# Optimization experiments

Hardware: AMD Instinct MI355X
Metric: run time of the kernel (lower is better)

Reference implementation:

```python
import jax, jax.numpy as jnp
import numpy as np

B, C, N = 2, 128, 4096
BN_EPS = 1e-5


def setup_inputs() -> dict:
    key = jax.random.key(0)
    ks = jax.random.split(key, 16)
    Ch, Cd = C // 2, C // 8

    def bn_params(k1, c):
        k1, k2 = jax.random.split(k1)
        return (1.0 + 0.1 * jax.random.normal(k1, (c,), jnp.float32),  # gamma
                0.1 * jax.random.normal(k2, (c,), jnp.float32),        # beta
                jnp.zeros((c,), jnp.float32),                          # running mean
                jnp.ones((c,), jnp.float32))                           # running var

    g1, be1, m1, v1 = bn_params(ks[4], Ch)
    g2, be2, m2, v2 = bn_params(ks[5], Ch)
    gu, beu, mu, vu = bn_params(ks[6], C)
    return {
        "xyz": jax.random.normal(ks[0], (B, 3, N), jnp.float32),
        "features": jax.random.normal(ks[1], (B, C, N), jnp.float32),
        "w_mlp1": 0.1 * jax.random.normal(ks[2], (Ch, 6), jnp.float32),
        "b_mlp1": jnp.zeros((Ch,), jnp.float32),
        "g_mlp1": g1, "be_mlp1": be1, "m_mlp1": m1, "v_mlp1": v1,
        "w_mlp2": 0.05 * jax.random.normal(ks[3], (Ch, 2 * C), jnp.float32),
        "b_mlp2": jnp.zeros((Ch,), jnp.float32),
        "g_mlp2": g2, "be_mlp2": be2, "m_mlp2": m2, "v_mlp2": v2,
        "w_down1": 0.1 * jax.random.normal(ks[7], (Cd, C), jnp.float32),
        "w_down2": 0.1 * jax.random.normal(ks[8], (Cd, C), jnp.float32),
        "w_up": 0.1 * jax.random.normal(ks[9], (C, Cd), jnp.float32),
        "b_up": jnp.zeros((C,), jnp.float32),
        "g_up": gu, "be_up": beu, "m_up": mu, "v_up": vu,
        "k": 20,
    }


def _knn_idx(x, k):
    # x: [B,3,N]; pairwise_distance = -||xi-xj||^2, topk -> nearest
    xx = jnp.sum(x * x, axis=1)                       # [B,N]
    inner = jnp.einsum('bcn,bcm->bnm', x, x)          # [B,N,N]
    pd = 2.0 * inner - xx[:, :, None] - xx[:, None, :]
    return jax.lax.top_k(pd, k)[1]                    # [B,N,k]


def _gather_edge(feat_t, idx):
    # feat_t: [B,N,C], idx: [B,N,k] -> concat(nbr - center, center): [B,N,k,2C]
    nbr = jax.vmap(lambda a, i: a[i])(feat_t, idx)    # [B,N,k,C]
    center = feat_t[:, :, None, :]
    center_b = jnp.broadcast_to(center, nbr.shape)
    return jnp.concatenate((nbr - center, center_b), axis=-1)


def _bn(x, g, b, m, v, ch_axis=1):
    shape = [1] * x.ndim
    shape[ch_axis] = -1
    r = lambda p: p.reshape(shape)
    return (x - r(m)) * (r(g) / jnp.sqrt(r(v) + BN_EPS)) + r(b)


def reference(xyz, features, w_mlp1, b_mlp1, g_mlp1, be_mlp1, m_mlp1, v_mlp1,
              w_mlp2, b_mlp2, g_mlp2, be_mlp2, m_mlp2, v_mlp2,
              w_down1, w_down2, w_up, b_up, g_up, be_up, m_up, v_up, k):
    idx = _knn_idx(xyz, k)
    edge_x = _gather_edge(jnp.swapaxes(xyz, 1, 2), idx)        # [B,N,k,6]
    edge_f = _gather_edge(jnp.swapaxes(features, 1, 2), idx)   # [B,N,k,2C]

    # 1x1 conv2d + BN + ReLU on both branches (channels last via einsum)
    h1 = jnp.einsum('bnkc,oc->bonk', edge_x, w_mlp1) + b_mlp1[None, :, None, None]
    h1 = jax.nn.relu(_bn(h1, g_mlp1, be_mlp1, m_mlp1, v_mlp1))
    h2 = jnp.einsum('bnkc,oc->bonk', edge_f, w_mlp2) + b_mlp2[None, :, None, None]
    h2 = jax.nn.relu(_bn(h2, g_mlp2, be_mlp2, m_mlp2, v_mlp2))

    f_enc = jnp.max(jnp.concatenate((h1, h2), axis=1), axis=-1)  # [B,C,N]

    f1 = jax.nn.relu(jnp.einsum('bcn,oc->bon', f_enc, w_down1))  # [B,C/8,N]
    f2 = jax.nn.relu(jnp.einsum('bcn,oc->bon', f_enc, w_down2))

    # NOTE: original code indexes [0] after mean -> uses batch element 0 only
    f_channel = jnp.mean(f1, axis=-1, keepdims=True)[0]          # [C/8,1]
    f_space = jnp.mean(f2, axis=1, keepdims=True)[0]             # [1,N]
    final = jnp.sqrt(f_channel @ f_space + 1e-12)                # [C/8,N]
    final = final[None] + f1 + f2                                # [B,C/8,N]

    up = jnp.einsum('bcn,oc->bon', final, w_up) + b_up[None, :, None]
    final = jax.nn.relu(_bn(up, g_up, be_up, m_up, v_up))        # [B,C,N]

    f_local = f_enc - final
    return f_local * jnp.tanh(jax.nn.softplus(f_local))          # Mish
```

## Files before the change

### kernel.cpp

```cpp
#include <hip/hip_runtime.h>
#include <hip/hip_bf16.h>

#define BB 2
#define CC 128
#define NN 4096
#define KK 20

#define WS_FLAG   0
#define WS_FCACC  16
#define WS_S1     32
#define WS_C1     96
#define WS_S2     160
#define WS_C2     224
#define WS_SUP    288
#define WS_CUP    416
#define WS_FS     1024
#define WS_X      8192
#define WS_XX     32768
#define WS_W1     40960
#define WS_W2     41344
#define WS_WD1    57728
#define WS_WD2    59776
#define WS_WUP    61824
#define WS_P      65536
#define WS_Q      1114112
#define WS_FE     2326528
#define WS_F      WS_FE
#define WS_F12    3375104

struct InPtrs { const void* p[22]; };

__device__ __forceinline__ int detect_bf16(const void* xyz) {
  const unsigned* u = (const unsigned*)xyz;
  int cnt = 0;
  for (int i = 0; i < 64; ++i) {
    unsigned lo = u[i] & 0x7FFFu;
    cnt += (lo >= 0x3C00u && lo <= 0x4100u) ? 1 : 0;
  }
  return cnt >= 32;
}

__device__ __forceinline__ float ldin(const void* p, long long i, int flag) {
  if (flag) {
    unsigned short b = ((const unsigned short*)p)[i];
    return __uint_as_float(((unsigned)b) << 16);
  }
  return ((const float*)p)[i];
}

__device__ __forceinline__ unsigned sortable(float v) {
  unsigned u = __float_as_uint(v);
  return (u & 0x80000000u) ? ~u : (u | 0x80000000u);
}

__device__ __forceinline__ unsigned wave_max_u32(unsigned x) {
  unsigned t;
  t = (unsigned)__builtin_amdgcn_update_dpp(0, (int)x, 0x111, 0xF, 0xF, true); x = x > t ? x : t;
  t = (unsigned)__builtin_amdgcn_update_dpp(0, (int)x, 0x112, 0xF, 0xF, true); x = x > t ? x : t;
  t = (unsigned)__builtin_amdgcn_update_dpp(0, (int)x, 0x114, 0xF, 0xF, true); x = x > t ? x : t;
  t = (unsigned)__builtin_amdgcn_update_dpp(0, (int)x, 0x118, 0xF, 0xF, true); x = x > t ? x : t;
  t = (unsigned)__builtin_amdgcn_update_dpp(0, (int)x, 0x142, 0xF, 0xF, true); x = x > t ? x : t;
  t = (unsigned)__builtin_amdgcn_update_dpp(0, (int)x, 0x143, 0xF, 0xF, true); x = x > t ? x : t;
  return (unsigned)__builtin_amdgcn_readlane((int)x, 63);
}

__device__ __forceinline__ void insert4p(unsigned pd, int idx,
    unsigned& p0, int& i0, unsigned& p1, int& i1,
    unsigned& p2, int& i2, unsigned& p3, int& i3) {
  bool b0 = pd > p0, b1 = pd > p1, b2 = pd > p2, b3 = pd > p3;
  p3 = b3 ? (b2 ? p2 : pd) : p3;  i3 = b3 ? (b2 ? i2 : idx) : i3;
  p2 = b2 ? (b1 ? p1 : pd) : p2;  i2 = b2 ? (b1 ? i1 : idx) : i2;
  p1 = b1 ? (b0 ? p0 : pd) : p1;  i1 = b1 ? (b0 ? i0 : idx) : i1;
  p0 = b0 ? pd : p0;              i0 = b0 ? idx : i0;
}

__global__ __launch_bounds__(256) void k0_convert(InPtrs in, float* ws) {
  int flag = detect_bf16(in.p[0]);
  int gid = blockIdx.x * 256 + threadIdx.x;
  int stride = gridDim.x * 256;
  if (flag) {
    const ushort4* src = (const ushort4*)in.p[1];
    float4* dst = (float4*)(ws + WS_F);
    for (int i = gid; i < 262144; i += stride) {
      ushort4 s = src[i];
      dst[i] = make_float4(
        __uint_as_float(((unsigned)s.x) << 16), __uint_as_float(((unsigned)s.y) << 16),
        __uint_as_float(((unsigned)s.z) << 16), __uint_as_float(((unsigned)s.w) << 16));
    }
  } else {
    const float4* src = (const float4*)in.p[1];
    float4* dst = (float4*)(ws + WS_F);
    for (int i = gid; i < 262144; i += stride) dst[i] = src[i];
  }
  const int T0 = 24576;
  const int T1 = T0 + 384;
  const int T2 = T1 + 16384;
  const int T3 = T2 + 2048;
  const int T4 = T3 + 2048;
  const int T5 = T4 + 2048;
  for (int i = gid; i < T5; i += stride) {
    const void* src; int off, dst;
    if      (i < T0) { src = in.p[0];  off = i;      dst = WS_X   + off; }
    else if (i < T1) { src = in.p[2];  off = i - T0; dst = WS_W1  + off; }
    else if (i < T2) { src = in.p[8];  off = i - T1; dst = WS_W2  + off; }
    else if (i < T3) { src = in.p[14]; off = i - T2; dst = WS_WD1 + off; }
    else if (i < T4) { src = in.p[15]; off = i - T3; dst = WS_WD2 + off; }
    else             { src = in.p[16]; off = i - T4; dst = WS_WUP + off; }
    ws[dst] = ldin(src, off, flag);
  }
  if (blockIdx.x == 0) {
    int t = threadIdx.x;
    if (t < 64) {
      float b1 = ldin(in.p[3], t, flag), g1 = ldin(in.p[4], t, flag);
      float be1 = ldin(in.p[5], t, flag), m1 = ldin(in.p[6], t, flag), v1 = ldin(in.p[7], t, flag);
      float s1 = g1 / sqrtf(v1 + 1e-5f);
      ws[WS_S1 + t] = s1;
      ws[WS_C1 + t] = s1 * (b1 - m1) + be1;
      float b2 = ldin(in.p[9], t, flag), g2 = ldin(in.p[10], t, flag);
      float be2 = ldin(in.p[11], t, flag), m2 = ldin(in.p[12], t, flag), v2 = ldin(in.p[13], t, flag);
      float s2 = g2 / sqrtf(v2 + 1e-5f);
      ws[WS_S2 + t] = s2;
      ws[WS_C2 + t] = s2 * (b2 - m2) + be2;
    }
    if (t < 128) {
      float bu = ldin(in.p[17], t, flag), gu = ldin(in.p[18], t, flag);
      float beu = ldin(in.p[19], t, flag), mu = ldin(in.p[20], t, flag), vu = ldin(in.p[21], t, flag);
      float su = gu / sqrtf(vu + 1e-5f);
      ws[WS_SUP + t] = su;
      ws[WS_CUP + t] = su * (bu - mu) + beu;
    }
    if (t < 16) ws[WS_FCACC + t] = 0.f;
    if (t == 0) ((int*)ws)[WS_FLAG] = flag;
  }
}

__global__ __launch_bounds__(256) void k1_pq(float* ws) {
  __shared__ float ldsW[64 * 128];
  __shared__ float ldsF[64 * 32];
  int t = threadIdx.x;
  int bid = blockIdx.x;
  int b = bid >> 7;
  int m0 = (bid & 127) << 5;
  int w = t >> 6, sub = (t >> 5) & 1, mloc = t & 31;
  const float* F = ws + WS_F + (long long)b * CC * NN;
  const float* W2 = ws + WS_W2;
  float accP[8], accQ[8];
#pragma unroll
  for (int j = 0; j < 8; ++j) { accP[j] = 0.f; accQ[j] = 0.f; }
  for (int half = 0; half < 2; ++half) {
    if (half) __syncthreads();
    for (int i = t; i < 64 * 128; i += 256) {
      int o = i >> 7, r = i & 127;
      int c = (r & 63) + half * 64 + ((r >> 6) << 7);
      ldsW[i] = W2[o * 256 + c];
    }
    for (int i = t; i < 64 * 32; i += 256) {
      int cl = i >> 5, ml = i & 31;
      ldsF[i] = F[(long long)(half * 64 + cl) * NN + m0 + ml];
    }
    __syncthreads();
    for (int cl = 0; cl < 64; ++cl) {
      float f = ldsF[cl * 32 + mloc];
#pragma unroll
      for (int j = 0; j < 8; ++j) {
        int o = w * 16 + sub * 8 + j;
        accP[j] = fmaf(ldsW[o * 128 + cl], f, accP[j]);
        accQ[j] = fmaf(ldsW[o * 128 + 64 + cl], f, accQ[j]);
      }
    }
  }
  int m = m0 + mloc;
  const float* X = ws + WS_X + (long long)b * 3 * NN;
  float x0 = X[m], x1 = X[NN + m], x2 = X[2 * NN + m];
  const float* W1 = ws + WS_W1;
  float* P = ws + WS_P + ((long long)(b * NN + m)) * 128;
  float* Q = ws + WS_Q + ((long long)(b * NN + m)) * 128;
#pragma unroll
  for (int j = 0; j < 8; ++j) {
    int o = w * 16 + sub * 8 + j;
    float s1 = ws[WS_S1 + o], c1 = ws[WS_C1 + o];
    float px = fmaf(W1[o * 6 + 2], x2, fmaf(W1[o * 6 + 1], x1, W1[o * 6 + 0] * x0));
    float qx = fmaf(W1[o * 6 + 5], x2, fmaf(W1[o * 6 + 4], x1, W1[o * 6 + 3] * x0));
    P[o] = s1 * px;
    Q[o] = fmaf(s1, qx - px, c1);
    float s2 = ws[WS_S2 + o], c2 = ws[WS_C2 + o];
    P[64 + o] = s2 * accP[j];
    Q[64 + o] = fmaf(s2, accQ[j] - accP[j], c2);
  }
  if (t < 32) {
    float xx = __fadd_rn(__fadd_rn(__fmul_rn(x0, x0), __fmul_rn(x1, x1)), __fmul_rn(x2, x2));
    ws[WS_XX + b * NN + m] = xx;
  }
}

__global__ __launch_bounds__(256) void k23_knn_fenc(float* ws) {
  int t = threadIdx.x;
  int w = t >> 6, lane = t & 63;
  int pt = blockIdx.x * 4 + w;
  int b = pt >> 12;
  int n = pt & (NN - 1);
  const float* X = ws + WS_X + (long long)b * 3 * NN;
  const float* XX = ws + WS_XX + (long long)b * NN;
  float xc0 = X[n], xc1 = X[NN + n], xc2 = X[2 * NN + n], xxn = XX[n];
  unsigned p0 = 0, p1 = 0, p2 = 0, p3 = 0;
  int i0 = 0, i1 = 0, i2 = 0, i3 = 0;
#pragma unroll 4
  for (int s = 0; s < 64; ++s) {
    int m = s * 64 + lane;
    float c0 = X[m], c1 = X[NN + m], c2 = X[2 * NN + m], xxm = XX[m];
    float inner = __fadd_rn(__fadd_rn(__fmul_rn(c0, xc0), __fmul_rn(c1, xc1)), __fmul_rn(c2, xc2));
    float pd = __fsub_rn(__fsub_rn(__fmul_rn(2.0f, inner), xxn), xxm);
    insert4p(sortable(pd), m, p0, i0, p1, i1, p2, i2, p3, i3);
  }
  unsigned long long used = 0;
  int nv = 4;
  int winner = 0;
  for (int r = 0; r < KK; ++r) {
    unsigned spd = wave_max_u32(p0);
    unsigned cand = (p0 == spd) ? (unsigned)(4095 - i0) : 0u;
    unsigned sidx = 4095u - wave_max_u32(cand);
    if (lane == r) winner = (int)sidx;
    if (p0 == spd && i0 == (int)sidx) {
      used |= 1ull << (i0 >> 6);
      p0 = p1; i0 = i1; p1 = p2; i1 = i2; p2 = p3; i2 = i3; p3 = 0; i3 = 0;
      if (--nv == 0) {
        p0 = p1 = p2 = p3 = 0; i0 = i1 = i2 = i3 = 0;
#pragma unroll 1
        for (int s = 0; s < 64; ++s) {
          if (!((used >> s) & 1ull)) {
            int m = s * 64 + lane;
            float c0 = X[m], c1 = X[NN + m], c2 = X[2 * NN + m], xxm = XX[m];
            float inner = __fadd_rn(__fadd_rn(__fmul_rn(c0, xc0), __fmul_rn(c1, xc1)), __fmul_rn(c2, xc2));
            float pd = __fsub_rn(__fsub_rn(__fmul_rn(2.0f, inner), xxn), xxm);
            insert4p(sortable(pd), m, p0, i0, p1, i1, p2, i2, p3, i3);
          }
        }
        nv = 4;
      }
    }
  }
  const float* Q = ws + WS_Q + (long long)pt * 128;
  const float* Pb = ws + WS_P + (long long)b * NN * 128;
  float2 q = ((const float2*)Q)[lane];
  float mx0 = -3.4e38f, mx1 = -3.4e38f;
#pragma unroll
  for (int j = 0; j < KK; ++j) {
    int id = __shfl(winner, j);
    float2 p = ((const float2*)(Pb + (long long)id * 128))[lane];
    mx0 = fmaxf(mx0, p.x + q.x);
    mx1 = fmaxf(mx1, p.y + q.y);
  }
  float2 fe = make_float2(fmaxf(mx0, 0.f), fmaxf(mx1, 0.f));
  ((float2*)(ws + WS_FE + (long long)pt * 128))[lane] = fe;
}

__global__ __launch_bounds__(256) void k4_down(float* ws) {
  __shared__ float ldsFE[8 * 128];
  __shared__ float ldsW[32 * 129];
  __shared__ float ldsFC[16];
  int t = threadIdx.x;
  int b = blockIdx.x >> 9;
  int n0 = (blockIdx.x & 511) << 3;
  for (int i = t; i < 8 * 128; i += 256) {
    int p = i >> 7, c = i & 127;
    ldsFE[i] = ws[WS_FE + (long long)(b * NN + n0 + p) * 128 + c];
  }
  for (int i = t; i < 32 * 128; i += 256) {
    int o = i >> 7, c = i & 127;
    ldsW[o * 129 + c] = (o < 16) ? ws[WS_WD1 + o * 128 + c] : ws[WS_WD2 + (o - 16) * 128 + c];
  }
  if (t < 16) ldsFC[t] = 0.f;
  __syncthreads();
  int p = t >> 5, oid = t & 31;
  float acc = 0.f;
#pragma unroll 8
  for (int c = 0; c < 128; ++c)
    acc = fmaf(ldsW[oid * 129 + c], ldsFE[p * 128 + c], acc);
  float v = fmaxf(acc, 0.f);
  ws[WS_F12 + (long long)(b * NN + n0 + p) * 32 + oid] = v;
  if (b == 0) {
    if (oid >= 16) {
      float s = v;
#pragma unroll
      for (int d = 1; d < 16; d <<= 1) s += __shfl_xor(s, d);
      if (oid == 16) ws[WS_FS + n0 + p] = s * 0.0625f;
    } else {
      atomicAdd(&ldsFC[oid], v);
    }
  }
  __syncthreads();
  if (b == 0 && t < 16) atomicAdd(ws + WS_FCACC + t, ldsFC[t]);
}

__global__ __launch_bounds__(256) void k5_final(float* ws, float* outf, __hip_bfloat16* outb) {
  __shared__ float fin[16 * 16];
  int t = threadIdx.x;
  int g = t >> 4;
  int p = t & 15;
  int b = blockIdx.x >> 8;
  int n0 = (blockIdx.x & 255) << 4;
  int n = n0 + p;
  int flag = ((const int*)ws)[WS_FLAG];
  {
    float fs = ws[WS_FS + n];
    float fc = ws[WS_FCACC + g] * (1.0f / NN);
    float f1v = ws[WS_F12 + (long long)(b * NN + n) * 32 + g];
    float f2v = ws[WS_F12 + (long long)(b * NN + n) * 32 + 16 + g];
    fin[p * 16 + g] = sqrtf(fc * fs + 1e-12f) + f1v + f2v;
  }
  __syncthreads();
  const float4* FE4 = (const float4*)(ws + WS_FE + (long long)(b * NN + n) * 128 + g * 8);
  float fev[8];
  {
    float4 a = FE4[0], c = FE4[1];
    fev[0] = a.x; fev[1] = a.y; fev[2] = a.z; fev[3] = a.w;
    fev[4] = c.x; fev[5] = c.y; fev[6] = c.z; fev[7] = c.w;
  }
#pragma unroll
  for (int j = 0; j < 8; ++j) {
    int o = g * 8 + j;
    float acc = 0.f;
#pragma unroll
    for (int c = 0; c < 16; ++c)
      acc = fmaf(ws[WS_WUP + o * 16 + c], fin[p * 16 + c], acc);
    float fo = fmaf(ws[WS_SUP + o], acc, ws[WS_CUP + o]);
    fo = fmaxf(fo, 0.f);
    float fl = fev[j] - fo;
    float u = __expf(fl);
    float nmr = u * (u + 2.f);
    float y = fl * __fdividef(nmr, nmr + 2.f);
    if (fl > 15.f) y = fl;
    long long oi = ((long long)b * CC + o) * NN + n;
    if (flag) outb[oi] = __float2bfloat16(y);
    else      outf[oi] = y;
  }
}

extern "C" void kernel_launch(void* const* d_in, const int* in_sizes, int n_in,
                              void* d_out, int out_size, void* d_ws, size_t ws_size,
                              hipStream_t stream) {
  (void)in_sizes; (void)out_size; (void)ws_size;
  float* ws = (float*)d_ws;
  InPtrs ip;
  for (int i = 0; i < 22; ++i) ip.p[i] = (i < n_in) ? d_in[i] : nullptr;
  hipLaunchKernelGGL(k0_convert,   dim3(512),          dim3(256), 0, stream, ip, ws);
  hipLaunchKernelGGL(k1_pq,        dim3(256),          dim3(256), 0, stream, ws);
  hipLaunchKernelGGL(k23_knn_fenc, dim3(BB * NN / 4),  dim3(256), 0, stream, ws);
  hipLaunchKernelGGL(k4_down,      dim3(BB * NN / 8),  dim3(256), 0, stream, ws);
  hipLaunchKernelGGL(k5_final,     dim3(BB * NN / 16), dim3(256), 0, stream, ws,
                     (float*)d_out, (__hip_bfloat16*)d_out);
}
```

Before: 209.0 us.

## Restructure k1_pq to drop LDS staging and use transposed W2

The conversion kernel now writes W2 in transposed layout so that each wave reads a contiguous run of output channels per input channel. k1_pq drops its shared-memory tiles and barriers. Each wave now computes 4 output channels for 64 points, with wave-uniform weight loads that can become scalar loads and feature loads that are coalesced. Results are written as float4 vectors, and the grid doubles to 512 blocks for more parallelism. In exchange, each block re-reads features from global memory instead of sharing them through LDS, since 4 blocks now read the same feature tile.

After: 201.4 us, median of 2. 3.6% less time.

```diff
diff --git a/kernel.cpp b/kernel.cpp
--- a/kernel.cpp
+++ b/kernel.cpp
@@ -18,7 +18,7 @@
 #define WS_X      8192
 #define WS_XX     32768
 #define WS_W1     40960
-#define WS_W2     41344
+#define WS_W2T    41344
 #define WS_WD1    57728
 #define WS_WD2    59776
 #define WS_WUP    61824
@@ -92,20 +92,22 @@
     float4* dst = (float4*)(ws + WS_F);
     for (int i = gid; i < 262144; i += stride) dst[i] = src[i];
   }
+  for (int i = gid; i < 16384; i += stride) {
+    int c = i >> 6, o = i & 63;
+    ws[WS_W2T + i] = ldin(in.p[8], o * 256 + c, flag);
+  }
   const int T0 = 24576;
   const int T1 = T0 + 384;
-  const int T2 = T1 + 16384;
+  const int T2 = T1 + 2048;
   const int T3 = T2 + 2048;
   const int T4 = T3 + 2048;
-  const int T5 = T4 + 2048;
-  for (int i = gid; i < T5; i += stride) {
+  for (int i = gid; i < T4; i += stride) {
     const void* src; int off, dst;
     if      (i < T0) { src = in.p[0];  off = i;      dst = WS_X   + off; }
     else if (i < T1) { src = in.p[2];  off = i - T0; dst = WS_W1  + off; }
-    else if (i < T2) { src = in.p[8];  off = i - T1; dst = WS_W2  + off; }
-    else if (i < T3) { src = in.p[14]; off = i - T2; dst = WS_WD1 + off; }
-    else if (i < T4) { src = in.p[15]; off = i - T3; dst = WS_WD2 + off; }
-    else             { src = in.p[16]; off = i - T4; dst = WS_WUP + off; }
+    else if (i < T2) { src = in.p[14]; off = i - T1; dst = WS_WD1 + off; }
+    else if (i < T3) { src = in.p[15]; off = i - T2; dst = WS_WD2 + off; }
+    else             { src = in.p[16]; off = i - T3; dst = WS_WUP + off; }
     ws[dst] = ldin(src, off, flag);
   }
   if (blockIdx.x == 0) {
@@ -135,59 +137,50 @@
 }
 
 __global__ __launch_bounds__(256) void k1_pq(float* ws) {
-  __shared__ float ldsW[64 * 128];
-  __shared__ float ldsF[64 * 32];
   int t = threadIdx.x;
   int bid = blockIdx.x;
-  int b = bid >> 7;
-  int m0 = (bid & 127) << 5;
-  int w = t >> 6, sub = (t >> 5) & 1, mloc = t & 31;
+  int b = bid >> 8;
+  int mt = (bid >> 2) & 63;
+  int ot = bid & 3;
+  int w = __builtin_amdgcn_readfirstlane(t >> 6);
+  int lane = t & 63;
+  int o0 = ot * 16 + w * 4;
+  int m = (mt << 6) + lane;
   const float* F = ws + WS_F + (long long)b * CC * NN;
-  const float* W2 = ws + WS_W2;
-  float accP[8], accQ[8];
-#pragma unroll
-  for (int j = 0; j < 8; ++j) { accP[j] = 0.f; accQ[j] = 0.f; }
-  for (int half = 0; half < 2; ++half) {
-    if (half) __syncthreads();
-    for (int i = t; i < 64 * 128; i += 256) {
-      int o = i >> 7, r = i & 127;
-      int c = (r & 63) + half * 64 + ((r >> 6) << 7);
-      ldsW[i] = W2[o * 256 + c];
-    }
-    for (int i = t; i < 64 * 32; i += 256) {
-      int cl = i >> 5, ml = i & 31;
-      ldsF[i] = F[(long long)(half * 64 + cl) * NN + m0 + ml];
-    }
-    __syncthreads();
-    for (int cl = 0; cl < 64; ++cl) {
-      float f = ldsF[cl * 32 + mloc];
-#pragma unroll
-      for (int j = 0; j < 8; ++j) {
-        int o = w * 16 + sub * 8 + j;
-        accP[j] = fmaf(ldsW[o * 128 + cl], f, accP[j]);
-        accQ[j] = fmaf(ldsW[o * 128 + 64 + cl], f, accQ[j]);
-      }
-    }
-  }
-  int m = m0 + mloc;
+  const float* W2T = ws + WS_W2T;
+  float accP[4] = {0.f, 0.f, 0.f, 0.f}, accQ[4] = {0.f, 0.f, 0.f, 0.f};
+#pragma unroll 4
+  for (int c = 0; c < 128; ++c) {
+    float f = F[c * NN + m];
+#pragma unroll
+    for (int j = 0; j < 4; ++j) {
+      accP[j] = fmaf(W2T[c * 64 + o0 + j], f, accP[j]);
+      accQ[j] = fmaf(W2T[(128 + c) * 64 + o0 + j], f, accQ[j]);
+    }
+  }
   const float* X = ws + WS_X + (long long)b * 3 * NN;
   float x0 = X[m], x1 = X[NN + m], x2 = X[2 * NN + m];
   const float* W1 = ws + WS_W1;
   float* P = ws + WS_P + ((long long)(b * NN + m)) * 128;
   float* Q = ws + WS_Q + ((long long)(b * NN + m)) * 128;
-#pragma unroll
-  for (int j = 0; j < 8; ++j) {
-    int o = w * 16 + sub * 8 + j;
+  float4 p1v, q1v, p2v, q2v;
+#pragma unroll
+  for (int j = 0; j < 4; ++j) {
+    int o = o0 + j;
     float s1 = ws[WS_S1 + o], c1 = ws[WS_C1 + o];
     float px = fmaf(W1[o * 6 + 2], x2, fmaf(W1[o * 6 + 1], x1, W1[o * 6 + 0] * x0));
     float qx = fmaf(W1[o * 6 + 5], x2, fmaf(W1[o * 6 + 4], x1, W1[o * 6 + 3] * x0));
-    P[o] = s1 * px;
-    Q[o] = fmaf(s1, qx - px, c1);
+    (&p1v.x)[j] = s1 * px;
+    (&q1v.x)[j] = fmaf(s1, qx - px, c1);
     float s2 = ws[WS_S2 + o], c2 = ws[WS_C2 + o];
-    P[64 + o] = s2 * accP[j];
-    Q[64 + o] = fmaf(s2, accQ[j] - accP[j], c2);
-  }
-  if (t < 32) {
+    (&p2v.x)[j] = s2 * accP[j];
+    (&q2v.x)[j] = fmaf(s2, accQ[j] - accP[j], c2);
+  }
+  *(float4*)(P + o0)      = p1v;
+  *(float4*)(P + 64 + o0) = p2v;
+  *(float4*)(Q + o0)      = q1v;
+  *(float4*)(Q + 64 + o0) = q2v;
+  if (ot == 0 && w == 0) {
     float xx = __fadd_rn(__fadd_rn(__fmul_rn(x0, x0), __fmul_rn(x1, x1)), __fmul_rn(x2, x2));
     ws[WS_XX + b * NN + m] = xx;
   }
@@ -344,7 +337,7 @@
   InPtrs ip;
   for (int i = 0; i < 22; ++i) ip.p[i] = (i < n_in) ? d_in[i] : nullptr;
   hipLaunchKernelGGL(k0_convert,   dim3(512),          dim3(256), 0, stream, ip, ws);
-  hipLaunchKernelGGL(k1_pq,        dim3(256),          dim3(256), 0, stream, ws);
+  hipLaunchKernelGGL(k1_pq,        dim3(512),          dim3(256), 0, stream, ws);
   hipLaunchKernelGGL(k23_knn_fenc, dim3(BB * NN / 4),  dim3(256), 0, stream, ws);
   hipLaunchKernelGGL(k4_down,      dim3(BB * NN / 8),  dim3(256), 0, stream, ws);
   hipLaunchKernelGGL(k5_final,     dim3(BB * NN / 16), dim3(256), 0, stream, ws,
```
